# Kernel tuning notes

Hardware: AMD Instinct MI355X
Metric: run time of the kernel (lower is better)

## Reference

```python
import jax, jax.numpy as jnp
import numpy as np
import math

HEADS = 32
GROUPS = 8
HEAD_DIM = 64
HIDDEN = 2048
B, S = 2, 2048


def _rope(x, freqs_cis):
    # x: (..., S, head_dim); freqs_cis: (S, head_dim) -> interleaved cos/sin pattern
    x_even = x[..., ::2]
    x_odd = x[..., 1::2]
    cos = freqs_cis[..., ::2]
    sin = freqs_cis[..., 1::2]
    r_even = x_even * cos - x_odd * sin
    r_odd = x_even * sin + x_odd * cos
    return jnp.stack([r_even, r_odd], axis=-1).reshape(x.shape)


def setup_inputs() -> dict:
    key = jax.random.key(0)
    ks = jax.random.split(key, 12)
    scale = 1.0 / math.sqrt(HIDDEN)
    x = jax.random.normal(ks[0], (B, S, HIDDEN), dtype=jnp.float32)
    freqs_cis = jax.random.uniform(ks[1], (S, HEAD_DIM), dtype=jnp.float32)
    causal = jnp.tril(jnp.ones((S, S), dtype=bool))
    mask = jnp.where(causal, 0.0, -1e9).astype(jnp.float32)
    kv_dims = HEAD_DIM * GROUPS
    wq = jax.random.normal(ks[2], (HIDDEN, HIDDEN), jnp.float32) * scale
    bq = jnp.zeros((HIDDEN,), jnp.float32)
    wk = jax.random.normal(ks[3], (kv_dims, HIDDEN), jnp.float32) * scale
    bk = jnp.zeros((kv_dims,), jnp.float32)
    wv = jax.random.normal(ks[4], (kv_dims, HIDDEN), jnp.float32) * scale
    bv = jnp.zeros((kv_dims,), jnp.float32)
    wo = jax.random.normal(ks[5], (HIDDEN, HIDDEN), jnp.float32) * scale
    bo = jnp.zeros((HIDDEN,), jnp.float32)
    return dict(x=x, freqs_cis=freqs_cis, mask=mask, wq=wq, bq=bq,
                wk=wk, bk=bk, wv=wv, bv=bv, wo=wo, bo=bo)


def reference(x, freqs_cis, mask, wq, bq, wk, bk, wv, bv, wo, bo):
    b, s, h = x.shape
    rep = HEADS // GROUPS
    q = x @ wq.T + bq                      # (B,S,H)
    k = x @ wk.T + bk                      # (B,S,G*hd)
    v = x @ wv.T + bv
    q = q.reshape(b, s, HEADS, HEAD_DIM).transpose(0, 2, 1, 3)   # (B,Hh,S,hd)
    k = k.reshape(b, s, GROUPS, HEAD_DIM).transpose(0, 2, 1, 3)  # (B,G,S,hd)
    v = v.reshape(b, s, GROUPS, HEAD_DIM).transpose(0, 2, 1, 3)
    q = _rope(q, freqs_cis)
    k = _rope(k, freqs_cis)
    # GQA: group q heads instead of materially repeating K/V
    qg = q.reshape(b, GROUPS, rep, s, HEAD_DIM)
    scores = jnp.einsum('bgrsd,bgtd->bgrst', qg, k) / math.sqrt(HEAD_DIM)
    scores = scores + mask                 # broadcast (S,S)
    attn = jax.nn.softmax(scores, axis=-1)
    out = jnp.einsum('bgrst,bgtd->bgrsd', attn, v)
    out = out.reshape(b, HEADS, s, HEAD_DIM).transpose(0, 2, 1, 3).reshape(b, s, h)
    return out @ wo.T + bo
```

## Files before the change

kernel.cpp:

```cpp
#include <hip/hip_runtime.h>

#define S_LEN 2048
#define HID   2048
#define NQH   32
#define NKV   8
#define HD    64

#define BM 256
#define BN 128
#define BK 64

typedef __bf16 bf16x8 __attribute__((ext_vector_type(8)));
typedef __bf16 bf16x4 __attribute__((ext_vector_type(4)));
typedef float  f32x4  __attribute__((ext_vector_type(4)));

#define MFMA16(a, b, c) __builtin_amdgcn_mfma_f32_16x16x32_bf16(a, b, c, 0, 0, 0)

__device__ __forceinline__ void async_copy16(const void* g, void* l) {
  __builtin_amdgcn_global_load_lds(
      (const __attribute__((address_space(1))) unsigned int*)g,
      (__attribute__((address_space(3))) unsigned int*)l, 16, 0, 0);
}

__global__ void cast_all_k(const float* __restrict__ x,  const float* __restrict__ wq,
                           const float* __restrict__ wk, const float* __restrict__ wv,
                           const float* __restrict__ wo,
                           __bf16* __restrict__ xb,  __bf16* __restrict__ wqb,
                           __bf16* __restrict__ wkb, __bf16* __restrict__ wvb,
                           __bf16* __restrict__ wob) {
  int bid = blockIdx.x;
  const float* in; __bf16* out; int base;
  if (bid < 8192)       { in = x;  out = xb;  base = bid; }
  else if (bid < 12288) { in = wq; out = wqb; base = bid - 8192; }
  else if (bid < 13312) { in = wk; out = wkb; base = bid - 12288; }
  else if (bid < 14336) { in = wv; out = wvb; base = bid - 13312; }
  else                  { in = wo; out = wob; base = bid - 14336; }
  int i = (base * 256 + threadIdx.x) * 4;
  float4 v = *(const float4*)(in + i);
  bf16x4 o;
  o[0] = (__bf16)v.x; o[1] = (__bf16)v.y; o[2] = (__bf16)v.z; o[3] = (__bf16)v.w;
  *(bf16x4*)(out + i) = o;
}

__device__ __forceinline__ void gemm_pipe(const __bf16* __restrict__ A,
                                          const __bf16* __restrict__ B,
                                          int m0, int n0, int K,
                                          __bf16 (&As)[3][BM][BK],
                                          __bf16 (&Bs)[3][BN][BK],
                                          f32x4 (&acc)[4][4]) {
  const int tid = threadIdx.x, wave = tid >> 6, lane = tid & 63;
  const int l15 = lane & 15, quad = lane >> 4;
  const int wr = wave >> 1, wc = wave & 1;

  const int srow = lane >> 3;
  const int scol = ((lane & 7) ^ srow) * 8;
  const __bf16* ga = A + (size_t)(m0 + wave * 32 + srow) * K + scol;
  const __bf16* gb = B + (size_t)(n0 + wave * 16 + srow) * K + scol;

  const int c0 = ((quad)     ^ (l15 & 7)) * 8;
  const int c1 = ((4 + quad) ^ (l15 & 7)) * 8;

  const int NT = K / BK;

#define STAGE(st, kt) do {                                                        \
    _Pragma("unroll")                                                             \
    for (int i = 0; i < 4; i++)                                                   \
      async_copy16(ga + (kt) + (size_t)(i * 8) * K, &As[st][wave * 32 + i * 8][0]); \
    _Pragma("unroll")                                                             \
    for (int i = 0; i < 2; i++)                                                   \
      async_copy16(gb + (kt) + (size_t)(i * 8) * K, &Bs[st][wave * 16 + i * 8][0]); \
  } while (0)

  STAGE(0, 0);
  STAGE(1, BK);

  int s = 0;
  for (int t = 0; t < NT; t++) {
    if (t + 1 < NT) asm volatile("s_waitcnt vmcnt(6) lgkmcnt(0)" ::: "memory");
    else            asm volatile("s_waitcnt vmcnt(0) lgkmcnt(0)" ::: "memory");
    __builtin_amdgcn_s_barrier();
    asm volatile("" ::: "memory");

    if (t + 2 < NT) {
      int s2 = s + 2; if (s2 >= 3) s2 -= 3;
      STAGE(s2, (t + 2) * BK);
    }

    const __bf16* a0 = &As[s][wr * 64][0];
    const __bf16* b0 = &Bs[s][wc * 64][0];
    bf16x8 af[2][4], bfr[2][4];
#pragma unroll
    for (int mt = 0; mt < 4; mt++) {
      af[0][mt] = *(const bf16x8*)(a0 + (mt * 16 + l15) * BK + c0);
      af[1][mt] = *(const bf16x8*)(a0 + (mt * 16 + l15) * BK + c1);
    }
#pragma unroll
    for (int nt = 0; nt < 4; nt++) {
      bfr[0][nt] = *(const bf16x8*)(b0 + (nt * 16 + l15) * BK + c0);
      bfr[1][nt] = *(const bf16x8*)(b0 + (nt * 16 + l15) * BK + c1);
    }

    __builtin_amdgcn_s_setprio(1);
#pragma unroll
    for (int kk = 0; kk < 2; kk++)
#pragma unroll
      for (int mt = 0; mt < 4; mt++)
#pragma unroll
        for (int nt = 0; nt < 4; nt++)
          acc[mt][nt] = MFMA16(af[kk][mt], bfr[kk][nt], acc[mt][nt]);
    __builtin_amdgcn_s_setprio(0);

    s = s + 1; if (s >= 3) s -= 3;
  }
#undef STAGE
}

__global__ __launch_bounds__(512, 2) void gemm_qkv_k(const __bf16* __restrict__ xb,
    const __bf16* __restrict__ wqb, const __bf16* __restrict__ wkb, const __bf16* __restrict__ wvb,
    const float* __restrict__ bq, const float* __restrict__ bk, const float* __restrict__ bv,
    const float* __restrict__ fr,
    __bf16* __restrict__ Qb, __bf16* __restrict__ Kb, __bf16* __restrict__ Vt) {
  __shared__ __align__(16) __bf16 As[3][BM][BK];
  __shared__ __align__(16) __bf16 Bs[3][BN][BK];
  const int by = blockIdx.y;
  const int m0 = blockIdx.x * BM;
  const __bf16* B; const float* bias; int n0;
  int mode;
  if (by < 16)      { B = wqb; bias = bq; n0 = by * 128;        mode = 0; }
  else if (by < 20) { B = wkb; bias = bk; n0 = (by - 16) * 128; mode = 1; }
  else              { B = wvb; bias = bv; n0 = (by - 20) * 128; mode = 2; }

  f32x4 acc[4][4] = {};
  gemm_pipe(xb, B, m0, n0, HID, As, Bs, acc);

  const int tid = threadIdx.x, wave = tid >> 6, lane = tid & 63;
  const int l15 = lane & 15, quad = lane >> 4;
  const int wr = wave >> 1, wc = wave & 1;

  if (mode == 2) {
#pragma unroll
    for (int nt = 0; nt < 4; nt++) {
      int col = n0 + wc * 64 + nt * 16 + l15;
      int g = col >> 6, d = col & 63;
      float bv2 = bias[col];
#pragma unroll
      for (int mt = 0; mt < 4; mt++) {
        int row = m0 + wr * 64 + mt * 16 + quad * 4;
        int b = row >> 11, sI = row & 2047;
        bf16x4 o;
#pragma unroll
        for (int r = 0; r < 4; r++) o[r] = (__bf16)(acc[mt][nt][r] + bv2);
        *(bf16x4*)(Vt + (((size_t)(b * NKV + g) * HD + d)) * S_LEN + sI) = o;
      }
    }
  } else {
    const float scale = (mode == 0) ? 0.125f * 1.44269504f : 1.0f;
    const int ldc = (mode == 0) ? HID : 512;
    __bf16* C = (mode == 0) ? Qb : Kb;
    const int dpar = l15 & 1;
#pragma unroll
    for (int nt = 0; nt < 4; nt++) {
      int col = n0 + wc * 64 + nt * 16 + l15;
      int d = col & 63;
      float bv2 = bias[col];
#pragma unroll
      for (int mt = 0; mt < 4; mt++) {
        int row = m0 + wr * 64 + mt * 16 + quad * 4;
        int sI = row & 2047;
#pragma unroll
        for (int r = 0; r < 4; r++) {
          float v = acc[mt][nt][r] + bv2;
          float p = __shfl_xor(v, 1, 64);
          float f = fr[(size_t)(sI + r) * HD + d];
          float fp = __shfl_xor(f, 1, 64);
          float o = dpar ? (p * f + v * fp) : (v * f - p * fp);
          C[(size_t)(row + r) * ldc + col] = (__bf16)(o * scale);
        }
      }
    }
  }
}

__global__ __launch_bounds__(512, 2) void gemm_out_k(const __bf16* __restrict__ A,
    const __bf16* __restrict__ Bw, const float* __restrict__ bias, float* __restrict__ C) {
  __shared__ __align__(16) __bf16 As[3][BM][BK];
  __shared__ __align__(16) __bf16 Bs[3][BN][BK];
  const int m0 = blockIdx.x * BM, n0 = blockIdx.y * BN;
  f32x4 acc[4][4] = {};
  gemm_pipe(A, Bw, m0, n0, HID, As, Bs, acc);
  const int tid = threadIdx.x, wave = tid >> 6, lane = tid & 63;
  const int l15 = lane & 15, quad = lane >> 4;
  const int wr = wave >> 1, wc = wave & 1;
#pragma unroll
  for (int nt = 0; nt < 4; nt++) {
    int col = n0 + wc * 64 + nt * 16 + l15;
    float bv = bias[col];
#pragma unroll
    for (int mt = 0; mt < 4; mt++) {
      int row = m0 + wr * 64 + mt * 16 + quad * 4;
#pragma unroll
      for (int r = 0; r < 4; r++)
        C[(size_t)(row + r) * HID + col] = acc[mt][nt][r] + bv;
    }
  }
}

__global__ __launch_bounds__(256, 4) void flash_k(const __bf16* __restrict__ Q,
                                                  const __bf16* __restrict__ K,
                                                  const __bf16* __restrict__ Vt,
                                                  __bf16* __restrict__ O) {
  __shared__ __align__(64) __bf16 Ksm[64][64];
  __shared__ __align__(64) __bf16 Vsm[64][64];
  __shared__ __align__(64) __bf16 Psm[4][16][64];
  const int tid = threadIdx.x;
  const int wave = tid >> 6, lane = tid & 63;
  const int l15 = lane & 15, quad = lane >> 4;
  const int x7 = l15 & 7, l15h = l15 >> 3;
  const int bh = blockIdx.x;
  const int b = bh >> 5, h = bh & 31, g = h >> 2;

  const int srow = tid >> 2, sc = (tid & 3) * 16;
  const int r7 = srow & 7;
  const int w0 = (((sc >> 3))     ^ r7) * 8;
  const int w1 = (((sc >> 3) + 1) ^ r7) * 8;

  char* kbp = (char*)&Ksm[0][0];
  char* vbp = (char*)&Vsm[0][0];
  char* pbp = (char*)&Psm[0][0][0];
  int kr[2], pr[2], pw[4];
#pragma unroll
  for (int ks = 0; ks < 2; ks++) {
    kr[ks] = l15 * 128 + (((ks * 4 + quad) ^ x7) * 16);
    pr[ks] = wave * 2048 + kr[ks];
  }
#pragma unroll
  for (int nt = 0; nt < 4; nt++)
    pw[nt] = wave * 2048 + quad * 512 + x7 * 2 + (((2 * nt + l15h) ^ ((quad & 1) * 4)) * 16);

  bf16x8 ones;
#pragma unroll
  for (int j = 0; j < 8; j++) ones[j] = (__bf16)1.0f;

  const __bf16* kbase = K + ((size_t)b * S_LEN + srow) * (NKV * HD) + g * HD + sc;
  const __bf16* vbase = Vt + (((size_t)b * NKV + g) * HD + srow) * S_LEN + sc;

#pragma unroll 1
  for (int half = 0; half < 2; half++) {
    const int qt = half ? (31 - (int)blockIdx.y) : (int)blockIdx.y;
    const int wq0 = qt * 64 + wave * 16;

    const __bf16* qp = Q + ((size_t)(b * S_LEN + wq0 + l15)) * HID + h * HD + quad * 8;
    bf16x8 qf0 = *(const bf16x8*)qp;
    bf16x8 qf1 = *(const bf16x8*)(qp + 32);

    f32x4 acc[4] = {};
    f32x4 accs = {};

    const __bf16* kp = kbase;
    const __bf16* vp = vbase;
    uint4 k0 = *(const uint4*)kp, k1 = *(const uint4*)(kp + 8);
    uint4 v0 = *(const uint4*)vp, v1 = *(const uint4*)(vp + 8);

    for (int t = 0; t <= qt; t++) {
      const int kv0 = t * 64;
      __syncthreads();
      *(uint4*)&Ksm[srow][w0] = k0;
      *(uint4*)&Ksm[srow][w1] = k1;
      *(uint4*)&Vsm[srow][w0] = v0;
      *(uint4*)&Vsm[srow][w1] = v1;
      if (t < qt) {
        kp += 64 * NKV * HD;  vp += 64;
        k0 = *(const uint4*)kp; k1 = *(const uint4*)(kp + 8);
        v0 = *(const uint4*)vp; v1 = *(const uint4*)(vp + 8);
      }
      __syncthreads();

      if (kv0 > wq0 + 15) continue;

      bf16x8 kf[2][4];
#pragma unroll
      for (int ks = 0; ks < 2; ks++)
#pragma unroll
        for (int nt = 0; nt < 4; nt++)
          kf[ks][nt] = *(const bf16x8*)(kbp + (kr[ks] + nt * 2048));

      f32x4 sacc[4] = {};
#pragma unroll
      for (int nt = 0; nt < 4; nt++) {
        sacc[nt] = MFMA16(qf0, kf[0][nt], sacc[nt]);
        sacc[nt] = MFMA16(qf1, kf[1][nt], sacc[nt]);
      }
      const bool domask = (kv0 + 63 > wq0);
#pragma unroll
      for (int nt = 0; nt < 4; nt++) {
        int kv = kv0 + nt * 16 + l15;
        int qr = wq0 + quad * 4;
#pragma unroll
        for (int r = 0; r < 4; r++) {
          float p = __builtin_exp2f(sacc[nt][r]);
          if (domask && kv > qr + r) p = 0.f;
          *(__bf16*)(pbp + ((pw[nt] ^ (r << 4)) + r * 128)) = (__bf16)p;
        }
      }

#pragma unroll
      for (int ks = 0; ks < 2; ks++) {
        bf16x8 vf[4];
#pragma unroll
        for (int nt = 0; nt < 4; nt++)
          vf[nt] = *(const bf16x8*)(vbp + (kr[ks] + nt * 2048));
        bf16x8 pf = *(const bf16x8*)(pbp + pr[ks]);
        accs = MFMA16(pf, ones, accs);
#pragma unroll
        for (int nt = 0; nt < 4; nt++)
          acc[nt] = MFMA16(pf, vf[nt], acc[nt]);
      }
    }

    __bf16* op = O + ((size_t)(b * S_LEN + wq0 + quad * 4)) * HID + h * HD;
    float inv[4];
#pragma unroll
    for (int r = 0; r < 4; r++) inv[r] = 1.f / accs[r];
#pragma unroll
    for (int nt = 0; nt < 4; nt++)
#pragma unroll
      for (int r = 0; r < 4; r++)
        op[(size_t)r * HID + nt * 16 + l15] = (__bf16)(acc[nt][r] * inv[r]);
  }
}

extern "C" void kernel_launch(void* const* d_in, const int* in_sizes, int n_in,
                              void* d_out, int out_size, void* d_ws, size_t ws_size,
                              hipStream_t stream) {
  (void)in_sizes; (void)n_in; (void)out_size; (void)ws_size;
  const float* x  = (const float*)d_in[0];
  const float* fr = (const float*)d_in[1];
  const float* wq = (const float*)d_in[3];
  const float* bq = (const float*)d_in[4];
  const float* wk = (const float*)d_in[5];
  const float* bk = (const float*)d_in[6];
  const float* wv = (const float*)d_in[7];
  const float* bv = (const float*)d_in[8];
  const float* wo = (const float*)d_in[9];
  const float* bo = (const float*)d_in[10];
  float* out = (float*)d_out;
  char* ws = (char*)d_ws;

  __bf16* xb  = (__bf16*)(ws);
  __bf16* wqb = (__bf16*)(ws + ((size_t)16 << 20));
  __bf16* wkb = (__bf16*)(ws + ((size_t)24 << 20));
  __bf16* wvb = (__bf16*)(ws + ((size_t)26 << 20));
  __bf16* wob = (__bf16*)(ws + ((size_t)28 << 20));
  __bf16* Qb  = (__bf16*)(ws + ((size_t)36 << 20));
  __bf16* Kb  = (__bf16*)(ws + ((size_t)52 << 20));
  __bf16* Vtb = (__bf16*)(ws + ((size_t)60 << 20));
  __bf16* Ab  = (__bf16*)(ws + ((size_t)64 << 20));

  cast_all_k<<<18432, 256, 0, stream>>>(x, wq, wk, wv, wo, xb, wqb, wkb, wvb, wob);

  gemm_qkv_k<<<dim3(16, 24), 512, 0, stream>>>(xb, wqb, wkb, wvb, bq, bk, bv, fr, Qb, Kb, Vtb);

  flash_k<<<dim3(64, 16), 256, 0, stream>>>(Qb, Kb, Vtb, Ab);

  gemm_out_k<<<dim3(16, 16), 512, 0, stream>>>(Ab, wob, bo, out);
}
```

Before: 339.8 us.

## Use 256x256 GEMM tiles with double buffering and barrier-interleaved MFMA phases

Enlarges the GEMM block tile from 256x128 to 256x256, switching from a 3-stage to a 2-stage LDS pipeline and a 2x4 wave layout where each wave computes 128x64. The MFMA loop is split into four barrier-separated phases that interleave A fragment loads with compute, in a ping-pong style schedule. The aim is more data reuse per LDS byte and fewer blocks. The cost is 64KB+64KB of LDS per block, which likely drops occupancy to one block per CU, plus only 192/128 blocks for the two GEMMs on a 256-CU part, which risks poor load balance.

New measurement: 372.4 us. 1.1x slower.

```diff
diff --git a/kernel.cpp b/kernel.cpp
--- a/kernel.cpp
+++ b/kernel.cpp
@@ -7,8 +7,9 @@
 #define HD    64
 
 #define BM 256
-#define BN 128
+#define BN 256
 #define BK 64
+#define NTILES (HID / BK)
 
 typedef __bf16 bf16x8 __attribute__((ext_vector_type(8)));
 typedef __bf16 bf16x4 __attribute__((ext_vector_type(4)));
@@ -21,6 +22,9 @@
       (const __attribute__((address_space(1))) unsigned int*)g,
       (__attribute__((address_space(3))) unsigned int*)l, 16, 0, 0);
 }
+
+#define FENCE asm volatile("" ::: "memory")
+#define BARRIER do { FENCE; __builtin_amdgcn_s_barrier(); FENCE; } while (0)
 
 __global__ void cast_all_k(const float* __restrict__ x,  const float* __restrict__ wq,
                            const float* __restrict__ wk, const float* __restrict__ wv,
@@ -45,74 +49,73 @@
 __device__ __forceinline__ void gemm_pipe(const __bf16* __restrict__ A,
                                           const __bf16* __restrict__ B,
                                           int m0, int n0, int K,
-                                          __bf16 (&As)[3][BM][BK],
-                                          __bf16 (&Bs)[3][BN][BK],
-                                          f32x4 (&acc)[4][4]) {
+                                          __bf16 (&As)[2][BM][BK],
+                                          __bf16 (&Bs)[2][BN][BK],
+                                          f32x4 (&acc)[8][4]) {
   const int tid = threadIdx.x, wave = tid >> 6, lane = tid & 63;
   const int l15 = lane & 15, quad = lane >> 4;
-  const int wr = wave >> 1, wc = wave & 1;
-
-  const int srow = lane >> 3;
-  const int scol = ((lane & 7) ^ srow) * 8;
-  const __bf16* ga = A + (size_t)(m0 + wave * 32 + srow) * K + scol;
-  const __bf16* gb = B + (size_t)(n0 + wave * 16 + srow) * K + scol;
+  const int wr = wave >> 2, wc = wave & 3;
+
+  const int srow8 = lane >> 3;
+  const int scol  = ((lane & 7) ^ srow8) * 8;
+  const __bf16* gA = A + (size_t)(m0 + wave * 8 + srow8) * K + scol;
+  const __bf16* gB = B + (size_t)(n0 + wave * 8 + srow8) * K + scol;
 
   const int c0 = ((quad)     ^ (l15 & 7)) * 8;
   const int c1 = ((4 + quad) ^ (l15 & 7)) * 8;
 
-  const int NT = K / BK;
-
-#define STAGE(st, kt) do {                                                        \
-    _Pragma("unroll")                                                             \
-    for (int i = 0; i < 4; i++)                                                   \
-      async_copy16(ga + (kt) + (size_t)(i * 8) * K, &As[st][wave * 32 + i * 8][0]); \
-    _Pragma("unroll")                                                             \
-    for (int i = 0; i < 2; i++)                                                   \
-      async_copy16(gb + (kt) + (size_t)(i * 8) * K, &Bs[st][wave * 16 + i * 8][0]); \
+#define STAGE8(sb, kt) do {                                                          \
+    _Pragma("unroll")                                                                \
+    for (int sw = 0; sw < 4; sw++)                                                   \
+      async_copy16(gA + (kt) + (size_t)(sw * 64) * K, &As[sb][sw * 64 + wave * 8][0]); \
+    _Pragma("unroll")                                                                \
+    for (int sw = 0; sw < 4; sw++)                                                   \
+      async_copy16(gB + (kt) + (size_t)(sw * 64) * K, &Bs[sb][sw * 64 + wave * 8][0]); \
   } while (0)
 
-  STAGE(0, 0);
-  STAGE(1, BK);
+  STAGE8(0, 0);
+  asm volatile("s_waitcnt vmcnt(0)" ::: "memory");
+  BARRIER;
 
   int s = 0;
-  for (int t = 0; t < NT; t++) {
-    if (t + 1 < NT) asm volatile("s_waitcnt vmcnt(6) lgkmcnt(0)" ::: "memory");
-    else            asm volatile("s_waitcnt vmcnt(0) lgkmcnt(0)" ::: "memory");
-    __builtin_amdgcn_s_barrier();
-    asm volatile("" ::: "memory");
-
-    if (t + 2 < NT) {
-      int s2 = s + 2; if (s2 >= 3) s2 -= 3;
-      STAGE(s2, (t + 2) * BK);
-    }
-
-    const __bf16* a0 = &As[s][wr * 64][0];
+#pragma unroll 1
+  for (int t = 0; t < NTILES; t++) {
+    const __bf16* a0 = &As[s][wr * 128][0];
     const __bf16* b0 = &Bs[s][wc * 64][0];
-    bf16x8 af[2][4], bfr[2][4];
-#pragma unroll
-    for (int mt = 0; mt < 4; mt++) {
-      af[0][mt] = *(const bf16x8*)(a0 + (mt * 16 + l15) * BK + c0);
-      af[1][mt] = *(const bf16x8*)(a0 + (mt * 16 + l15) * BK + c1);
-    }
+
+    if (t + 1 < NTILES) STAGE8(s ^ 1, (t + 1) * BK);
+
+    bf16x8 bfr[4][2], af[2][2];
 #pragma unroll
     for (int nt = 0; nt < 4; nt++) {
-      bfr[0][nt] = *(const bf16x8*)(b0 + (nt * 16 + l15) * BK + c0);
-      bfr[1][nt] = *(const bf16x8*)(b0 + (nt * 16 + l15) * BK + c1);
-    }
-
-    __builtin_amdgcn_s_setprio(1);
-#pragma unroll
-    for (int kk = 0; kk < 2; kk++)
-#pragma unroll
-      for (int mt = 0; mt < 4; mt++)
+      bfr[nt][0] = *(const bf16x8*)(b0 + (nt * 16 + l15) * BK + c0);
+      bfr[nt][1] = *(const bf16x8*)(b0 + (nt * 16 + l15) * BK + c1);
+    }
+
+#pragma unroll
+    for (int mp = 0; mp < 4; mp++) {
+#pragma unroll
+      for (int m2 = 0; m2 < 2; m2++) {
+        af[m2][0] = *(const bf16x8*)(a0 + ((mp * 2 + m2) * 16 + l15) * BK + c0);
+        af[m2][1] = *(const bf16x8*)(a0 + ((mp * 2 + m2) * 16 + l15) * BK + c1);
+      }
+      if (mp == 3 && t + 1 < NTILES)
+        asm volatile("s_waitcnt vmcnt(0)" ::: "memory");
+      BARRIER;
+      __builtin_amdgcn_s_setprio(1);
+#pragma unroll
+      for (int m2 = 0; m2 < 2; m2++)
 #pragma unroll
         for (int nt = 0; nt < 4; nt++)
-          acc[mt][nt] = MFMA16(af[kk][mt], bfr[kk][nt], acc[mt][nt]);
-    __builtin_amdgcn_s_setprio(0);
-
-    s = s + 1; if (s >= 3) s -= 3;
-  }
-#undef STAGE
+#pragma unroll
+          for (int kk = 0; kk < 2; kk++)
+            acc[mp * 2 + m2][nt] = MFMA16(af[m2][kk], bfr[nt][kk], acc[mp * 2 + m2][nt]);
+      __builtin_amdgcn_s_setprio(0);
+      BARRIER;
+    }
+    s ^= 1;
+  }
+#undef STAGE8
 }
 
 __global__ __launch_bounds__(512, 2) void gemm_qkv_k(const __bf16* __restrict__ xb,
@@ -120,22 +123,22 @@
     const float* __restrict__ bq, const float* __restrict__ bk, const float* __restrict__ bv,
     const float* __restrict__ fr,
     __bf16* __restrict__ Qb, __bf16* __restrict__ Kb, __bf16* __restrict__ Vt) {
-  __shared__ __align__(16) __bf16 As[3][BM][BK];
-  __shared__ __align__(16) __bf16 Bs[3][BN][BK];
+  __shared__ __align__(16) __bf16 As[2][BM][BK];
+  __shared__ __align__(16) __bf16 Bs[2][BN][BK];
   const int by = blockIdx.y;
   const int m0 = blockIdx.x * BM;
   const __bf16* B; const float* bias; int n0;
   int mode;
-  if (by < 16)      { B = wqb; bias = bq; n0 = by * 128;        mode = 0; }
-  else if (by < 20) { B = wkb; bias = bk; n0 = (by - 16) * 128; mode = 1; }
-  else              { B = wvb; bias = bv; n0 = (by - 20) * 128; mode = 2; }
-
-  f32x4 acc[4][4] = {};
+  if (by < 8)       { B = wqb; bias = bq; n0 = by * 256;        mode = 0; }
+  else if (by < 10) { B = wkb; bias = bk; n0 = (by - 8) * 256;  mode = 1; }
+  else              { B = wvb; bias = bv; n0 = (by - 10) * 256; mode = 2; }
+
+  f32x4 acc[8][4] = {};
   gemm_pipe(xb, B, m0, n0, HID, As, Bs, acc);
 
   const int tid = threadIdx.x, wave = tid >> 6, lane = tid & 63;
   const int l15 = lane & 15, quad = lane >> 4;
-  const int wr = wave >> 1, wc = wave & 1;
+  const int wr = wave >> 2, wc = wave & 3;
 
   if (mode == 2) {
 #pragma unroll
@@ -144,8 +147,8 @@
       int g = col >> 6, d = col & 63;
       float bv2 = bias[col];
 #pragma unroll
-      for (int mt = 0; mt < 4; mt++) {
-        int row = m0 + wr * 64 + mt * 16 + quad * 4;
+      for (int mt = 0; mt < 8; mt++) {
+        int row = m0 + wr * 128 + mt * 16 + quad * 4;
         int b = row >> 11, sI = row & 2047;
         bf16x4 o;
 #pragma unroll
@@ -164,8 +167,8 @@
       int d = col & 63;
       float bv2 = bias[col];
 #pragma unroll
-      for (int mt = 0; mt < 4; mt++) {
-        int row = m0 + wr * 64 + mt * 16 + quad * 4;
+      for (int mt = 0; mt < 8; mt++) {
+        int row = m0 + wr * 128 + mt * 16 + quad * 4;
         int sI = row & 2047;
 #pragma unroll
         for (int r = 0; r < 4; r++) {
@@ -183,21 +186,21 @@
 
 __global__ __launch_bounds__(512, 2) void gemm_out_k(const __bf16* __restrict__ A,
     const __bf16* __restrict__ Bw, const float* __restrict__ bias, float* __restrict__ C) {
-  __shared__ __align__(16) __bf16 As[3][BM][BK];
-  __shared__ __align__(16) __bf16 Bs[3][BN][BK];
+  __shared__ __align__(16) __bf16 As[2][BM][BK];
+  __shared__ __align__(16) __bf16 Bs[2][BN][BK];
   const int m0 = blockIdx.x * BM, n0 = blockIdx.y * BN;
-  f32x4 acc[4][4] = {};
+  f32x4 acc[8][4] = {};
   gemm_pipe(A, Bw, m0, n0, HID, As, Bs, acc);
   const int tid = threadIdx.x, wave = tid >> 6, lane = tid & 63;
   const int l15 = lane & 15, quad = lane >> 4;
-  const int wr = wave >> 1, wc = wave & 1;
+  const int wr = wave >> 2, wc = wave & 3;
 #pragma unroll
   for (int nt = 0; nt < 4; nt++) {
     int col = n0 + wc * 64 + nt * 16 + l15;
     float bv = bias[col];
 #pragma unroll
-    for (int mt = 0; mt < 4; mt++) {
-      int row = m0 + wr * 64 + mt * 16 + quad * 4;
+    for (int mt = 0; mt < 8; mt++) {
+      int row = m0 + wr * 128 + mt * 16 + quad * 4;
 #pragma unroll
       for (int r = 0; r < 4; r++)
         C[(size_t)(row + r) * HID + col] = acc[mt][nt][r] + bv;
@@ -358,9 +361,9 @@
 
   cast_all_k<<<18432, 256, 0, stream>>>(x, wq, wk, wv, wo, xb, wqb, wkb, wvb, wob);
 
-  gemm_qkv_k<<<dim3(16, 24), 512, 0, stream>>>(xb, wqb, wkb, wvb, bq, bk, bv, fr, Qb, Kb, Vtb);
+  gemm_qkv_k<<<dim3(16, 12), 512, 0, stream>>>(xb, wqb, wkb, wvb, bq, bk, bv, fr, Qb, Kb, Vtb);
 
   flash_k<<<dim3(64, 16), 256, 0, stream>>>(Qb, Kb, Vtb, Ab);
 
-  gemm_out_k<<<dim3(16, 16), 512, 0, stream>>>(Ab, wob, bo, out);
-}
+  gemm_out_k<<<dim3(16, 8), 512, 0, stream>>>(Ab, wob, bo, out);
+}
```
